# Optimization experiments

Hardware: AMD Instinct MI355X
Metric: run time of the kernel (lower is better)

The kernel has to match this reference:

```python
import jax, jax.numpy as jnp
import numpy as np
from jax import lax

N_NODES = 100000
D = 2048
E = 8192
H = 128
SIM_THRESHOLD = 0.7
EPS = 1e-8  # torch CosineSimilarity default eps


def setup_inputs() -> dict:
    key = jax.random.key(0)
    ks = jax.random.split(key, 8)
    x_idx = jax.random.randint(ks[0], (E,), 0, N_NODES, dtype=jnp.int32)
    y_idx = jax.random.randint(ks[1], (E,), 0, N_NODES, dtype=jnp.int32)
    x_feat = jax.random.normal(ks[2], (E, D), dtype=jnp.float32)
    y_feat = jax.random.normal(ks[3], (E, D), dtype=jnp.float32)
    # make ~half the pairs highly similar so the sim >= 0.7 branch is exercised
    coin = jax.random.uniform(ks[4], (E, 1)) < 0.5
    y_feat = jnp.where(coin, x_feat + 0.5 * y_feat, y_feat)
    W1 = 0.02 * jax.random.normal(ks[5], (H, 2 * D), dtype=jnp.float32)
    b1 = jnp.zeros((H,), jnp.float32)
    W2 = 0.02 * jax.random.normal(ks[6], (1, H), dtype=jnp.float32)
    b2 = jnp.zeros((1,), jnp.float32)
    parent = jnp.arange(N_NODES, dtype=jnp.int32)
    rank = jnp.ones((N_NODES,), jnp.float32)
    return {"x_idx": x_idx, "y_idx": y_idx, "x_feat": x_feat, "y_feat": y_feat,
            "W1": W1, "b1": b1, "W2": W2, "b2": b2,
            "parent": parent, "rank": rank}


def _gate(x_feat, y_feat, W1, b1, W2, b2):
    # cosine similarity with torch's eps clamp on each norm
    dot = jnp.sum(x_feat * y_feat, axis=-1)
    nx = jnp.maximum(jnp.sqrt(jnp.sum(x_feat * x_feat, axis=-1)), EPS)
    ny = jnp.maximum(jnp.sqrt(jnp.sum(y_feat * y_feat, axis=-1)), EPS)
    sim = dot / (nx * ny)
    h = jax.nn.relu(jnp.concatenate([x_feat, y_feat], axis=-1) @ W1.T + b1)  # [E, H]
    attn = jax.nn.sigmoid(h @ W2.T + b2)[:, 0]                               # [E]
    mask = sim >= SIM_THRESHOLD
    w = jnp.where(mask, attn, jnp.zeros_like(attn))
    return w, mask


def _find_root(parent, i):
    # iterative root find
    root = lax.while_loop(lambda r: parent[r] != r, lambda r: parent[r], i)
    # path compression: point every node on the path at root (matches recursive torch find)
    def comp_body(state):
        p, j = state
        nj = p[j]
        p = p.at[j].set(root)
        return p, nj
    parent, _ = lax.while_loop(lambda s: s[1] != root, comp_body, (parent, i))
    return parent, root


def reference(x_idx, y_idx, x_feat, y_feat, W1, b1, W2, b2, parent, rank):
    w, mask = _gate(x_feat, y_feat, W1, b1, W2, b2)

    def step(carry, inp):
        x, y, wi, m = inp
        def do(c):
            p, r = c
            p, rx = _find_root(p, x)
            p, ry = _find_root(p, y)
            bigger_x = r[rx] > r[ry]
            big = jnp.where(bigger_x, rx, ry)
            small = jnp.where(bigger_x, ry, rx)
            same = rx == ry
            # if roots are equal: no structural change, no rank update
            p = p.at[jnp.where(same, big, small)].set(big)
            r = r.at[big].add(jnp.where(same, 0.0, r[small] * wi))
            return p, r
        carry = lax.cond(m, do, lambda c: c, carry)
        return carry, None

    (parent, rank), _ = lax.scan(step, (parent, rank), (x_idx, y_idx, w, mask))
    return w, parent, rank
```

## Files before the change

kernel.cpp:

```cpp
#include <hip/hip_runtime.h>
#include <math.h>

#define E_EDGES 8192
#define D_FEAT 2048
#define K2 4096
#define H_DIM 128
#define N_NODES 100000
#define SIM_TH 0.7f
#define NSLOTS (2 * E_EDGES)
#define GBM 16

__global__ __launch_bounds__(256) void sim_kernel(const float* __restrict__ xf,
                                                  const float* __restrict__ yf,
                                                  float* __restrict__ sim) {
    int gid  = blockIdx.x * blockDim.x + threadIdx.x;
    int wave = gid >> 6;
    int lane = threadIdx.x & 63;
    if (wave >= E_EDGES) return;
    const float4* xp = (const float4*)(xf + (size_t)wave * D_FEAT);
    const float4* yp = (const float4*)(yf + (size_t)wave * D_FEAT);
    float dot = 0.f, xx = 0.f, yy = 0.f;
#pragma unroll
    for (int j = 0; j < 8; ++j) {
        float4 a = xp[lane + j * 64];
        float4 b = yp[lane + j * 64];
        dot += a.x * b.x + a.y * b.y + a.z * b.z + a.w * b.w;
        xx  += a.x * a.x + a.y * a.y + a.z * a.z + a.w * a.w;
        yy  += b.x * b.x + b.y * b.y + b.z * b.z + b.w * b.w;
    }
#pragma unroll
    for (int off = 32; off; off >>= 1) {
        dot += __shfl_xor(dot, off);
        xx  += __shfl_xor(xx, off);
        yy  += __shfl_xor(yy, off);
    }
    if (lane == 0) {
        float nx = fmaxf(sqrtf(xx), 1e-8f);
        float ny = fmaxf(sqrtf(yy), 1e-8f);
        sim[wave] = dot / (nx * ny);
    }
}

__global__ void initmap_kernel(int* __restrict__ fo, int* __restrict__ orig,
                               float* __restrict__ wout) {
    int i = blockIdx.x * blockDim.x + threadIdx.x;
    if (i < N_NODES) fo[i] = 0x7FFFFFFF;
    if (i < NSLOTS)  orig[i] = -1;
    if (i < E_EDGES) wout[i] = 0.f;
}

__global__ void claim_kernel(const int* __restrict__ x_idx, const int* __restrict__ y_idx,
                             int* __restrict__ fo) {
    int i = blockIdx.x * blockDim.x + threadIdx.x;
    if (i >= NSLOTS) return;
    int e = i >> 1;
    int v = (i & 1) ? y_idx[e] : x_idx[e];
    atomicMin(&fo[v], i);
}

__global__ void orig_kernel(const int* __restrict__ x_idx, const int* __restrict__ y_idx,
                            const int* __restrict__ fo, int* __restrict__ orig) {
    int i = blockIdx.x * blockDim.x + threadIdx.x;
    if (i >= NSLOTS) return;
    int e = i >> 1;
    int v = (i & 1) ? y_idx[e] : x_idx[e];
    if (fo[v] == i) orig[i] = v;
}

__global__ __launch_bounds__(256) void maskscan_kernel(
        const int* __restrict__ x_idx, const int* __restrict__ y_idx,
        const int* __restrict__ fo, const float* __restrict__ sim,
        int4* __restrict__ rec, int* __restrict__ nmask) {
    __shared__ int partial[256];
    int t = threadIdx.x;
    int cnt = 0;
    for (int j = 0; j < 32; ++j) {
        int e = t * 32 + j;
        cnt += (sim[e] >= SIM_TH) ? 1 : 0;
    }
    partial[t] = cnt;
    __syncthreads();
    for (int off = 1; off < 256; off <<= 1) {
        int mine  = partial[t];
        int other = (t >= off) ? partial[t - off] : 0;
        __syncthreads();
        partial[t] = mine + other;
        __syncthreads();
    }
    int pos = partial[t] - cnt;
    if (t == 255) {
        int nn = partial[255];
        *nmask = nn;
        for (int j = 0; j < 4; ++j) rec[nn + j] = make_int4(0, 0, 0, 0);
    }
    for (int j = 0; j < 32; ++j) {
        int e = t * 32 + j;
        if (sim[e] >= SIM_TH) {
            int4 r;
            r.x = fo[x_idx[e]];
            r.y = fo[y_idx[e]];
            r.z = e;
            r.w = 0;
            rec[pos++] = r;
        }
    }
}

__global__ __launch_bounds__(256) void gate_split_kernel(
        const float* __restrict__ xf, const float* __restrict__ yf,
        const float* __restrict__ W1,
        const int4* __restrict__ rec, const int* __restrict__ nmask,
        float* __restrict__ pbuf) {
    __shared__ float As[2][GBM][32];
    __shared__ float Bs[2][H_DIM][33];
    __shared__ int   elds[GBM];

    int n  = *nmask;
    int b0 = blockIdx.x * GBM;
    if (b0 >= n) return;
    const int h = blockIdx.y;

    int t = threadIdx.x;
    if (t < GBM) {
        int idx = b0 + t;
        elds[t] = (idx < n) ? rec[idx].z : rec[b0].z;
    }
    __syncthreads();

    const int  arow = t >> 3;
    const int  acol = (t & 7) * 4;
    const bool aact = (t < 128);
    const int  brow = t >> 3;
    const int  bcol = (t & 7) * 4;

    const float* feat = h ? yf : xf;
    const float* arp  = feat + (size_t)elds[aact ? arow : 0] * D_FEAT + acol;
    const size_t koff = (size_t)h * D_FEAT;
    const float* w1p0 = W1 + (size_t)(brow +  0) * K2 + koff + bcol;
    const float* w1p1 = W1 + (size_t)(brow + 32) * K2 + koff + bcol;
    const float* w1p2 = W1 + (size_t)(brow + 64) * K2 + koff + bcol;
    const float* w1p3 = W1 + (size_t)(brow + 96) * K2 + koff + bcol;

    float4 aR = make_float4(0.f, 0.f, 0.f, 0.f);
    float4 bR0, bR1, bR2, bR3;

    if (aact) aR = *(const float4*)(arp + 0);
    bR0 = *(const float4*)(w1p0 + 0);
    bR1 = *(const float4*)(w1p1 + 0);
    bR2 = *(const float4*)(w1p2 + 0);
    bR3 = *(const float4*)(w1p3 + 0);
    if (aact) *(float4*)(&As[0][arow][acol]) = aR;
    Bs[0][brow +  0][bcol + 0] = bR0.x; Bs[0][brow +  0][bcol + 1] = bR0.y;
    Bs[0][brow +  0][bcol + 2] = bR0.z; Bs[0][brow +  0][bcol + 3] = bR0.w;
    Bs[0][brow + 32][bcol + 0] = bR1.x; Bs[0][brow + 32][bcol + 1] = bR1.y;
    Bs[0][brow + 32][bcol + 2] = bR1.z; Bs[0][brow + 32][bcol + 3] = bR1.w;
    Bs[0][brow + 64][bcol + 0] = bR2.x; Bs[0][brow + 64][bcol + 1] = bR2.y;
    Bs[0][brow + 64][bcol + 2] = bR2.z; Bs[0][brow + 64][bcol + 3] = bR2.w;
    Bs[0][brow + 96][bcol + 0] = bR3.x; Bs[0][brow + 96][bcol + 1] = bR3.y;
    Bs[0][brow + 96][bcol + 2] = bR3.z; Bs[0][brow + 96][bcol + 3] = bR3.w;
    __syncthreads();

    const int eb = (t >> 6) * 4;
    const int ln = t & 63;
    float acc[4][2] = {{0.f,0.f},{0.f,0.f},{0.f,0.f},{0.f,0.f}};

    const int NT = D_FEAT / 32;
    for (int tile = 0; tile < NT; ++tile) {
        const int buf = tile & 1;
        if (tile + 1 < NT) {
            int k0 = (tile + 1) * 32;
            if (aact) aR = *(const float4*)(arp + k0);
            bR0 = *(const float4*)(w1p0 + k0);
            bR1 = *(const float4*)(w1p1 + k0);
            bR2 = *(const float4*)(w1p2 + k0);
            bR3 = *(const float4*)(w1p3 + k0);
        }
#pragma unroll
        for (int kk = 0; kk < 32; kk += 4) {
            float4 a0 = *(const float4*)(&As[buf][eb + 0][kk]);
            float4 a1 = *(const float4*)(&As[buf][eb + 1][kk]);
            float4 a2 = *(const float4*)(&As[buf][eb + 2][kk]);
            float4 a3 = *(const float4*)(&As[buf][eb + 3][kk]);
            float bl0 = Bs[buf][ln][kk + 0];
            float bl1 = Bs[buf][ln][kk + 1];
            float bl2 = Bs[buf][ln][kk + 2];
            float bl3 = Bs[buf][ln][kk + 3];
            float bh0 = Bs[buf][ln + 64][kk + 0];
            float bh1 = Bs[buf][ln + 64][kk + 1];
            float bh2 = Bs[buf][ln + 64][kk + 2];
            float bh3 = Bs[buf][ln + 64][kk + 3];
            acc[0][0] = fmaf(a0.x, bl0, acc[0][0]);
            acc[0][0] = fmaf(a0.y, bl1, acc[0][0]);
            acc[0][0] = fmaf(a0.z, bl2, acc[0][0]);
            acc[0][0] = fmaf(a0.w, bl3, acc[0][0]);
            acc[0][1] = fmaf(a0.x, bh0, acc[0][1]);
            acc[0][1] = fmaf(a0.y, bh1, acc[0][1]);
            acc[0][1] = fmaf(a0.z, bh2, acc[0][1]);
            acc[0][1] = fmaf(a0.w, bh3, acc[0][1]);
            acc[1][0] = fmaf(a1.x, bl0, acc[1][0]);
            acc[1][0] = fmaf(a1.y, bl1, acc[1][0]);
            acc[1][0] = fmaf(a1.z, bl2, acc[1][0]);
            acc[1][0] = fmaf(a1.w, bl3, acc[1][0]);
            acc[1][1] = fmaf(a1.x, bh0, acc[1][1]);
            acc[1][1] = fmaf(a1.y, bh1, acc[1][1]);
            acc[1][1] = fmaf(a1.z, bh2, acc[1][1]);
            acc[1][1] = fmaf(a1.w, bh3, acc[1][1]);
            acc[2][0] = fmaf(a2.x, bl0, acc[2][0]);
            acc[2][0] = fmaf(a2.y, bl1, acc[2][0]);
            acc[2][0] = fmaf(a2.z, bl2, acc[2][0]);
            acc[2][0] = fmaf(a2.w, bl3, acc[2][0]);
            acc[2][1] = fmaf(a2.x, bh0, acc[2][1]);
            acc[2][1] = fmaf(a2.y, bh1, acc[2][1]);
            acc[2][1] = fmaf(a2.z, bh2, acc[2][1]);
            acc[2][1] = fmaf(a2.w, bh3, acc[2][1]);
            acc[3][0] = fmaf(a3.x, bl0, acc[3][0]);
            acc[3][0] = fmaf(a3.y, bl1, acc[3][0]);
            acc[3][0] = fmaf(a3.z, bl2, acc[3][0]);
            acc[3][0] = fmaf(a3.w, bl3, acc[3][0]);
            acc[3][1] = fmaf(a3.x, bh0, acc[3][1]);
            acc[3][1] = fmaf(a3.y, bh1, acc[3][1]);
            acc[3][1] = fmaf(a3.z, bh2, acc[3][1]);
            acc[3][1] = fmaf(a3.w, bh3, acc[3][1]);
        }
        if (tile + 1 < NT) {
            const int nb = buf ^ 1;
            if (aact) *(float4*)(&As[nb][arow][acol]) = aR;
            Bs[nb][brow +  0][bcol + 0] = bR0.x; Bs[nb][brow +  0][bcol + 1] = bR0.y;
            Bs[nb][brow +  0][bcol + 2] = bR0.z; Bs[nb][brow +  0][bcol + 3] = bR0.w;
            Bs[nb][brow + 32][bcol + 0] = bR1.x; Bs[nb][brow + 32][bcol + 1] = bR1.y;
            Bs[nb][brow + 32][bcol + 2] = bR1.z; Bs[nb][brow + 32][bcol + 3] = bR1.w;
            Bs[nb][brow + 64][bcol + 0] = bR2.x; Bs[nb][brow + 64][bcol + 1] = bR2.y;
            Bs[nb][brow + 64][bcol + 2] = bR2.z; Bs[nb][brow + 64][bcol + 3] = bR2.w;
            Bs[nb][brow + 96][bcol + 0] = bR3.x; Bs[nb][brow + 96][bcol + 1] = bR3.y;
            Bs[nb][brow + 96][bcol + 2] = bR3.z; Bs[nb][brow + 96][bcol + 3] = bR3.w;
        }
        __syncthreads();
    }

#pragma unroll
    for (int j = 0; j < 4; ++j) {
        float* pb = pbuf + (((size_t)(b0 + eb + j) * 2 + h) << 7);
        pb[ln]      = acc[j][0];
        pb[ln + 64] = acc[j][1];
    }
}

__global__ __launch_bounds__(256) void gate_fin_kernel(
        const float* __restrict__ pbuf, const float* __restrict__ b1,
        const float* __restrict__ W2, const float* __restrict__ b2,
        int4* __restrict__ rec, const int* __restrict__ nmask,
        float* __restrict__ wout) {
    int e = blockIdx.x * blockDim.x + threadIdx.x;
    if (e >= *nmask) return;
    const float* p0 = pbuf + ((size_t)e << 8);
    const float* p1 = p0 + 128;
    float s = 0.f;
    for (int c = 0; c < 32; ++c) {
        float p = 0.f;
#pragma unroll
        for (int q = 0; q < 4; ++q) {
            int nn = 4 * c + q;
            float hh = fmaxf(p0[nn] + p1[nn] + b1[nn], 0.f);
            p = fmaf(hh, W2[nn], p);
        }
        s += p;
    }
    float logit = s + b2[0];
    float attn  = 1.f / (1.f + expf(-logit));
    wout[rec[e].z] = attn;
    ((int*)&rec[e])[3] = __float_as_int(attn);
}

__global__ __launch_bounds__(256) void gate_v3_kernel(
        const float* __restrict__ xf, const float* __restrict__ yf,
        const float* __restrict__ W1, const float* __restrict__ b1,
        const float* __restrict__ W2, const float* __restrict__ b2,
        int4* __restrict__ rec, const int* __restrict__ nmask,
        float* __restrict__ wout) {
    __shared__ float As[2][GBM][32];
    __shared__ float Bs[2][H_DIM][33];
    __shared__ float hbuf[GBM][132];
    __shared__ int   elds[GBM];

    int n  = *nmask;
    int b0 = blockIdx.x * GBM;
    if (b0 >= n) return;

    int t = threadIdx.x;
    if (t < GBM) {
        int idx = b0 + t;
        elds[t] = (idx < n) ? rec[idx].z : rec[b0].z;
    }
    __syncthreads();

    const int  arow = t >> 3;
    const int  acol = (t & 7) * 4;
    const bool aact = (t < 128);
    const int  brow = t >> 3;
    const int  bcol = (t & 7) * 4;

    const float* xrow = xf + (size_t)elds[aact ? arow : 0] * D_FEAT + acol;
    const float* yrow = yf + (size_t)elds[aact ? arow : 0] * D_FEAT + acol;
    const float* w1p0 = W1 + (size_t)(brow +  0) * K2 + bcol;
    const float* w1p1 = W1 + (size_t)(brow + 32) * K2 + bcol;
    const float* w1p2 = W1 + (size_t)(brow + 64) * K2 + bcol;
    const float* w1p3 = W1 + (size_t)(brow + 96) * K2 + bcol;

    float4 aR = make_float4(0.f, 0.f, 0.f, 0.f);
    float4 bR0, bR1, bR2, bR3;

    if (aact) aR = *(const float4*)(xrow + 0);
    bR0 = *(const float4*)(w1p0 + 0);
    bR1 = *(const float4*)(w1p1 + 0);
    bR2 = *(const float4*)(w1p2 + 0);
    bR3 = *(const float4*)(w1p3 + 0);
    if (aact) *(float4*)(&As[0][arow][acol]) = aR;
    Bs[0][brow +  0][bcol + 0] = bR0.x; Bs[0][brow +  0][bcol + 1] = bR0.y;
    Bs[0][brow +  0][bcol + 2] = bR0.z; Bs[0][brow +  0][bcol + 3] = bR0.w;
    Bs[0][brow + 32][bcol + 0] = bR1.x; Bs[0][brow + 32][bcol + 1] = bR1.y;
    Bs[0][brow + 32][bcol + 2] = bR1.z; Bs[0][brow + 32][bcol + 3] = bR1.w;
    Bs[0][brow + 64][bcol + 0] = bR2.x; Bs[0][brow + 64][bcol + 1] = bR2.y;
    Bs[0][brow + 64][bcol + 2] = bR2.z; Bs[0][brow + 64][bcol + 3] = bR2.w;
    Bs[0][brow + 96][bcol + 0] = bR3.x; Bs[0][brow + 96][bcol + 1] = bR3.y;
    Bs[0][brow + 96][bcol + 2] = bR3.z; Bs[0][brow + 96][bcol + 3] = bR3.w;
    __syncthreads();

    const int eb = (t >> 6) * 4;
    const int ln = t & 63;
    float acc[4][2] = {{0.f,0.f},{0.f,0.f},{0.f,0.f},{0.f,0.f}};

    const int NT = K2 / 32;
    for (int tile = 0; tile < NT; ++tile) {
        const int buf = tile & 1;
        if (tile + 1 < NT) {
            int k0 = (tile + 1) * 32;
            if (aact) {
                const float* ap = (k0 < D_FEAT) ? (xrow + k0) : (yrow + (k0 - D_FEAT));
                aR = *(const float4*)ap;
            }
            bR0 = *(const float4*)(w1p0 + k0);
            bR1 = *(const float4*)(w1p1 + k0);
            bR2 = *(const float4*)(w1p2 + k0);
            bR3 = *(const float4*)(w1p3 + k0);
        }
#pragma unroll
        for (int kk = 0; kk < 32; kk += 4) {
            float4 a0 = *(const float4*)(&As[buf][eb + 0][kk]);
            float4 a1 = *(const float4*)(&As[buf][eb + 1][kk]);
            float4 a2 = *(const float4*)(&As[buf][eb + 2][kk]);
            float4 a3 = *(const float4*)(&As[buf][eb + 3][kk]);
            float bl0 = Bs[buf][ln][kk + 0];
            float bl1 = Bs[buf][ln][kk + 1];
            float bl2 = Bs[buf][ln][kk + 2];
            float bl3 = Bs[buf][ln][kk + 3];
            float bh0 = Bs[buf][ln + 64][kk + 0];
            float bh1 = Bs[buf][ln + 64][kk + 1];
            float bh2 = Bs[buf][ln + 64][kk + 2];
            float bh3 = Bs[buf][ln + 64][kk + 3];
            acc[0][0] = fmaf(a0.x, bl0, acc[0][0]);
            acc[0][0] = fmaf(a0.y, bl1, acc[0][0]);
            acc[0][0] = fmaf(a0.z, bl2, acc[0][0]);
            acc[0][0] = fmaf(a0.w, bl3, acc[0][0]);
            acc[0][1] = fmaf(a0.x, bh0, acc[0][1]);
            acc[0][1] = fmaf(a0.y, bh1, acc[0][1]);
            acc[0][1] = fmaf(a0.z, bh2, acc[0][1]);
            acc[0][1] = fmaf(a0.w, bh3, acc[0][1]);
            acc[1][0] = fmaf(a1.x, bl0, acc[1][0]);
            acc[1][0] = fmaf(a1.y, bl1, acc[1][0]);
            acc[1][0] = fmaf(a1.z, bl2, acc[1][0]);
            acc[1][0] = fmaf(a1.w, bl3, acc[1][0]);
            acc[1][1] = fmaf(a1.x, bh0, acc[1][1]);
            acc[1][1] = fmaf(a1.y, bh1, acc[1][1]);
            acc[1][1] = fmaf(a1.z, bh2, acc[1][1]);
            acc[1][1] = fmaf(a1.w, bh3, acc[1][1]);
            acc[2][0] = fmaf(a2.x, bl0, acc[2][0]);
            acc[2][0] = fmaf(a2.y, bl1, acc[2][0]);
            acc[2][0] = fmaf(a2.z, bl2, acc[2][0]);
            acc[2][0] = fmaf(a2.w, bl3, acc[2][0]);
            acc[2][1] = fmaf(a2.x, bh0, acc[2][1]);
            acc[2][1] = fmaf(a2.y, bh1, acc[2][1]);
            acc[2][1] = fmaf(a2.z, bh2, acc[2][1]);
            acc[2][1] = fmaf(a2.w, bh3, acc[2][1]);
            acc[3][0] = fmaf(a3.x, bl0, acc[3][0]);
            acc[3][0] = fmaf(a3.y, bl1, acc[3][0]);
            acc[3][0] = fmaf(a3.z, bl2, acc[3][0]);
            acc[3][0] = fmaf(a3.w, bl3, acc[3][0]);
            acc[3][1] = fmaf(a3.x, bh0, acc[3][1]);
            acc[3][1] = fmaf(a3.y, bh1, acc[3][1]);
            acc[3][1] = fmaf(a3.z, bh2, acc[3][1]);
            acc[3][1] = fmaf(a3.w, bh3, acc[3][1]);
        }
        if (tile + 1 < NT) {
            const int nb = buf ^ 1;
            if (aact) *(float4*)(&As[nb][arow][acol]) = aR;
            Bs[nb][brow +  0][bcol + 0] = bR0.x; Bs[nb][brow +  0][bcol + 1] = bR0.y;
            Bs[nb][brow +  0][bcol + 2] = bR0.z; Bs[nb][brow +  0][bcol + 3] = bR0.w;
            Bs[nb][brow + 32][bcol + 0] = bR1.x; Bs[nb][brow + 32][bcol + 1] = bR1.y;
            Bs[nb][brow + 32][bcol + 2] = bR1.z; Bs[nb][brow + 32][bcol + 3] = bR1.w;
            Bs[nb][brow + 64][bcol + 0] = bR2.x; Bs[nb][brow + 64][bcol + 1] = bR2.y;
            Bs[nb][brow + 64][bcol + 2] = bR2.z; Bs[nb][brow + 64][bcol + 3] = bR2.w;
            Bs[nb][brow + 96][bcol + 0] = bR3.x; Bs[nb][brow + 96][bcol + 1] = bR3.y;
            Bs[nb][brow + 96][bcol + 2] = bR3.z; Bs[nb][brow + 96][bcol + 3] = bR3.w;
        }
        __syncthreads();
    }

#pragma unroll
    for (int j = 0; j < 4; ++j) {
        hbuf[eb + j][ln]      = fmaxf(acc[j][0] + b1[ln], 0.f);
        hbuf[eb + j][ln + 64] = fmaxf(acc[j][1] + b1[ln + 64], 0.f);
    }
    __syncthreads();
    if (t < GBM && b0 + t < n) {
        float s = 0.f;
        for (int c = 0; c < 32; ++c) {
            float p = 0.f;
#pragma unroll
            for (int q = 0; q < 4; ++q)
                p = fmaf(hbuf[t][4 * c + q], W2[4 * c + q], p);
            s += p;
        }
        float logit = s + b2[0];
        float attn  = 1.f / (1.f + expf(-logit));
        wout[elds[t]] = attn;
        ((int*)&rec[b0 + t])[3] = __float_as_int(attn);
    }
}

__global__ __launch_bounds__(1024) void label_kernel(
        const int4* __restrict__ rec, const int* __restrict__ nmask,
        int* __restrict__ elab) {
    extern __shared__ int L[];
    int t = threadIdx.x;
    int n = *nmask;
    for (int c = t; c < NSLOTS; c += 1024) L[c] = c;
    __syncthreads();
    for (;;) {
        if (t == 0) L[NSLOTS] = 0;
        __syncthreads();
        for (int e = t; e < n; e += 1024) {
            int4 r = rec[e];
            int a = L[r.x], b = L[r.y];
            if (a < b)      { atomicMin(&L[r.y], a); L[NSLOTS] = 1; }
            else if (b < a) { atomicMin(&L[r.x], b); L[NSLOTS] = 1; }
        }
        __syncthreads();
        if (!L[NSLOTS]) break;
        __syncthreads();
        for (int c = t; c < NSLOTS; c += 1024) {
            int q  = L[c];
            int qq = L[q];
            if (qq < q) L[c] = qq;
        }
        __syncthreads();
    }
    __syncthreads();
    for (int e = t; e < n; e += 1024) elab[e] = L[rec[e].x];
}

__global__ __launch_bounds__(1024) void radix_kernel(
        int4* __restrict__ bufA, int4* __restrict__ bufB,
        int* __restrict__ keyA, int* __restrict__ keyB,
        const int* __restrict__ nmask,
        int* __restrict__ compStart, int* __restrict__ ncompOut) {
    __shared__ int F[16384];
    __shared__ int P[1024];
    int t = threadIdx.x;
    int n = *nmask;
    int c = (n + 1023) >> 10;

    for (int pass = 0; pass < 4; ++pass) {
        int sh = pass * 4;
        const int4* in   = (pass & 1) ? bufB : bufA;
        int4*       out  = (pass & 1) ? bufA : bufB;
        const int*  kin  = (pass & 1) ? keyB : keyA;
        int*        kout = (pass & 1) ? keyA : keyB;
        for (int q = 0; q < 16; ++q) F[t * 16 + q] = 0;
        __syncthreads();
        for (int j = 0; j < c; ++j) {
            int i = t * c + j;
            if (i < n) {
                int d = (kin[i] >> sh) & 15;
                F[d * 1024 + t] += 1;
            }
        }
        __syncthreads();
        int base = t * 16;
        int loc[16]; int s = 0;
#pragma unroll
        for (int q = 0; q < 16; ++q) { loc[q] = s; s += F[base + q]; }
        P[t] = s;
        __syncthreads();
        for (int off = 1; off < 1024; off <<= 1) {
            int mine  = P[t];
            int other = (t >= off) ? P[t - off] : 0;
            __syncthreads();
            P[t] = mine + other;
            __syncthreads();
        }
        int pre = (t == 0) ? 0 : P[t - 1];
#pragma unroll
        for (int q = 0; q < 16; ++q) F[base + q] = pre + loc[q];
        __syncthreads();
        for (int j = 0; j < c; ++j) {
            int i = t * c + j;
            if (i < n) {
                int k = kin[i];
                int d = (k >> sh) & 15;
                int pos = F[d * 1024 + t]++;
                out[pos]  = in[i];
                kout[pos] = k;
            }
        }
        __syncthreads();
    }

    unsigned char* hd = (unsigned char*)F;
    for (int i = t; i < n; i += 1024) {
        int l  = keyA[i];
        int lp = (i == 0) ? -1 : keyA[i - 1];
        hd[i] = (l != lp) ? 1 : 0;
    }
    __syncthreads();
    int hsum = 0;
    for (int j = 0; j < c; ++j) {
        int i = t * c + j;
        if (i < n) hsum += hd[i];
    }
    P[t] = hsum;
    __syncthreads();
    for (int off = 1; off < 1024; off <<= 1) {
        int mine  = P[t];
        int other = (t >= off) ? P[t - off] : 0;
        __syncthreads();
        P[t] = mine + other;
        __syncthreads();
    }
    int run = P[t] - hsum;
    for (int j = 0; j < c; ++j) {
        int i = t * c + j;
        if (i < n && hd[i]) { compStart[run] = i; ++run; }
    }
    if (t == 1023) { int total = P[1023]; *ncompOut = total; compStart[total] = n; }
}

__global__ __launch_bounds__(1024) void uf_kernel(
        const int4* __restrict__ srec, const int* __restrict__ ncompPtr,
        const int* __restrict__ compStart,
        const int* __restrict__ orig, const float* __restrict__ rin,
        int* __restrict__ gpar, float* __restrict__ grank) {
    extern __shared__ char smem[];
    int2* nd = (int2*)smem;
    int* ndw = (int*)smem;
    int t = threadIdx.x;
    for (int c = t; c < NSLOTS; c += 1024) {
        int o = orig[c];
        float r = (o >= 0) ? rin[o] : 1.0f;
        nd[c] = make_int2(c, __float_as_int(r));
    }
    __syncthreads();

    int ncomp = *ncompPtr;
    for (int c = t; c < ncomp; c += 1024) {
        int s  = compStart[c];
        int en = compStart[c + 1];
        for (int j = s; j < en; ++j) {
            int4 r = srec[j];
            int x = r.x, y = r.y;
            float wi = __int_as_float(r.w);
            int p;
            int rx = x;
            while ((p = ndw[rx * 2]) != rx) rx = p;
            int j2 = x;
            while ((p = ndw[j2 * 2]) != rx) { ndw[j2 * 2] = rx; j2 = p; }
            int ry = y;
            while ((p = ndw[ry * 2]) != ry) ry = p;
            j2 = y;
            while ((p = ndw[j2 * 2]) != ry) { ndw[j2 * 2] = ry; j2 = p; }
            if (rx != ry) {
                float ka = __int_as_float(ndw[rx * 2 + 1]);
                float kb = __int_as_float(ndw[ry * 2 + 1]);
                bool bx = ka > kb;
                int big = bx ? rx : ry, small = bx ? ry : rx;
                float nr = bx ? (ka + kb * wi) : (kb + ka * wi);
                ndw[small * 2]   = big;
                ndw[big * 2 + 1] = __float_as_int(nr);
            }
        }
    }
    __syncthreads();
    for (int c = t; c < NSLOTS; c += 1024) {
        int2 v = nd[c];
        gpar[c] = v.x;
        grank[c] = __int_as_float(v.y);
    }
}

__global__ void finalize_kernel(const int* __restrict__ pin, const float* __restrict__ rin,
                                const int* __restrict__ fo, const int* __restrict__ orig,
                                const int* __restrict__ gpar, const float* __restrict__ grank,
                                float* __restrict__ pout, float* __restrict__ rout) {
    int i = blockIdx.x * blockDim.x + threadIdx.x;
    if (i >= N_NODES) return;
    int c = fo[i];
    float pv, rv;
    if (c != 0x7FFFFFFF) {
        pv = (float)orig[gpar[c]];
        rv = grank[c];
    } else {
        pv = (float)pin[i];
        rv = rin[i];
    }
    pout[i] = pv;
    rout[i] = rv;
}

extern "C" void kernel_launch(void* const* d_in, const int* in_sizes, int n_in,
                              void* d_out, int out_size, void* d_ws, size_t ws_size,
                              hipStream_t stream) {
    const int*   x_idx = (const int*)d_in[0];
    const int*   y_idx = (const int*)d_in[1];
    const float* xf    = (const float*)d_in[2];
    const float* yf    = (const float*)d_in[3];
    const float* W1    = (const float*)d_in[4];
    const float* b1    = (const float*)d_in[5];
    const float* W2    = (const float*)d_in[6];
    const float* b2    = (const float*)d_in[7];
    const int*   pin   = (const int*)d_in[8];
    const float* rin   = (const float*)d_in[9];

    float* out   = (float*)d_out;
    float* w_out = out;
    float* pout  = out + E_EDGES;
    float* rout  = out + E_EDGES + N_NODES;

    char* ws = (char*)d_ws;
    float* sim_ws  = (float*)(ws + 0);
    int*   fo      = (int*)  (ws + 32768);
    int*   orig    = (int*)  (ws + 432768);
    int4*  rec     = (int4*) (ws + 498304);
    int*   nmask   = (int*)  (ws + 629440);
    int*   gpar    = (int*)  (ws + 629504);
    float* grank   = (float*)(ws + 695040);
    int4*  srec    = (int4*) (ws + 760576);
    int*   keyB    = (int*)  (ws + 891648);
    int*   compSt  = (int*)  (ws + 924416);
    int*   ncomp   = (int*)  (ws + 957188);
    float* pbuf    = (float*)(ws + 957440);
    int*   keyA    = (int*)sim_ws;

    const size_t need_split = 957440 + (size_t)E_EDGES * 256 * sizeof(float);

    sim_kernel<<<(E_EDGES * 64) / 256, 256, 0, stream>>>(xf, yf, sim_ws);
    int g = (N_NODES + 255) / 256;
    initmap_kernel<<<g, 256, 0, stream>>>(fo, orig, w_out);
    claim_kernel<<<NSLOTS / 256, 256, 0, stream>>>(x_idx, y_idx, fo);
    orig_kernel<<<NSLOTS / 256, 256, 0, stream>>>(x_idx, y_idx, fo, orig);
    maskscan_kernel<<<1, 256, 0, stream>>>(x_idx, y_idx, fo, sim_ws, rec, nmask);
    if (ws_size >= need_split) {
        dim3 gg(E_EDGES / GBM, 2);
        gate_split_kernel<<<gg, 256, 0, stream>>>(xf, yf, W1, rec, nmask, pbuf);
        gate_fin_kernel<<<E_EDGES / 256, 256, 0, stream>>>(pbuf, b1, W2, b2,
                                                           rec, nmask, w_out);
    } else {
        gate_v3_kernel<<<E_EDGES / GBM, 256, 0, stream>>>(xf, yf, W1, b1, W2, b2,
                                                          rec, nmask, w_out);
    }
    label_kernel<<<1, 1024, (NSLOTS + 1) * sizeof(int), stream>>>(rec, nmask, keyA);
    radix_kernel<<<1, 1024, 0, stream>>>(rec, srec, keyA, keyB, nmask, compSt, ncomp);
    uf_kernel<<<1, 1024, 131072, stream>>>(rec, ncomp, compSt, orig, rin, gpar, grank);
    finalize_kernel<<<g, 256, 0, stream>>>(pin, rin, fo, orig, gpar, grank, pout, rout);
}
```

Baseline: 267.8 us.

## Fuse mask compaction, component labeling and radix sort into one kernel

Merges the mask-scan, label-propagation and radix-sort kernels into a single 1024-thread block. That block keeps the sort keys and label array in LDS instead of global memory, and it now runs before the gate GEMM. The aim is to cut two kernel launches and the global round-trips of the key and label arrays on this serial single-block path. It needs about 136 KB of dynamic LDS. The gate now works on records already sorted by component, and it still writes each attention value back into its record.

```diff
diff --git a/kernel.cpp b/kernel.cpp
--- a/kernel.cpp
+++ b/kernel.cpp
@@ -67,34 +67,44 @@
     if (fo[v] == i) orig[i] = v;
 }
 
-__global__ __launch_bounds__(256) void maskscan_kernel(
+__global__ __launch_bounds__(1024) void sortprep_kernel(
         const int* __restrict__ x_idx, const int* __restrict__ y_idx,
         const int* __restrict__ fo, const float* __restrict__ sim,
-        int4* __restrict__ rec, int* __restrict__ nmask) {
-    __shared__ int partial[256];
+        int4* __restrict__ rec, int4* __restrict__ srec,
+        int* __restrict__ nmask, int* __restrict__ compStart,
+        int* __restrict__ ncompOut) {
+    extern __shared__ char sm[];
+    int* keys0 = (int*)sm;
+    int* keys1 = (int*)(sm + 32768);
+    int* C     = (int*)(sm + 65536);
+    int* P     = (int*)(sm + 131072);
     int t = threadIdx.x;
+
     int cnt = 0;
-    for (int j = 0; j < 32; ++j) {
-        int e = t * 32 + j;
+#pragma unroll
+    for (int j = 0; j < 8; ++j) {
+        int e = t * 8 + j;
         cnt += (sim[e] >= SIM_TH) ? 1 : 0;
     }
-    partial[t] = cnt;
-    __syncthreads();
-    for (int off = 1; off < 256; off <<= 1) {
-        int mine  = partial[t];
-        int other = (t >= off) ? partial[t - off] : 0;
-        __syncthreads();
-        partial[t] = mine + other;
-        __syncthreads();
-    }
-    int pos = partial[t] - cnt;
-    if (t == 255) {
-        int nn = partial[255];
-        *nmask = nn;
+    P[t] = cnt;
+    __syncthreads();
+    for (int off = 1; off < 1024; off <<= 1) {
+        int mine  = P[t];
+        int other = (t >= off) ? P[t - off] : 0;
+        __syncthreads();
+        P[t] = mine + other;
+        __syncthreads();
+    }
+    int pos = P[t] - cnt;
+    if (t == 1023) {
+        int nn = P[1023];
+        *nmask  = nn;
+        P[1501] = nn;
         for (int j = 0; j < 4; ++j) rec[nn + j] = make_int4(0, 0, 0, 0);
     }
-    for (int j = 0; j < 32; ++j) {
-        int e = t * 32 + j;
+#pragma unroll
+    for (int j = 0; j < 8; ++j) {
+        int e = t * 8 + j;
         if (sim[e] >= SIM_TH) {
             int4 r;
             r.x = fo[x_idx[e]];
@@ -104,6 +114,111 @@
             rec[pos++] = r;
         }
     }
+    __syncthreads();
+    const int n = P[1501];
+
+    int* L = C;
+    for (int c = t; c < NSLOTS; c += 1024) L[c] = c;
+    __syncthreads();
+    for (;;) {
+        if (t == 0) P[1500] = 0;
+        __syncthreads();
+        for (int e = t; e < n; e += 1024) {
+            int4 r = rec[e];
+            int a = L[r.x], b = L[r.y];
+            if (a < b)      { atomicMin(&L[r.y], a); P[1500] = 1; }
+            else if (b < a) { atomicMin(&L[r.x], b); P[1500] = 1; }
+        }
+        __syncthreads();
+        if (!P[1500]) break;
+        __syncthreads();
+        for (int c = t; c < NSLOTS; c += 1024) {
+            int q  = L[c];
+            int qq = L[q];
+            if (qq < q) L[c] = qq;
+        }
+        __syncthreads();
+    }
+    __syncthreads();
+    for (int e = t; e < n; e += 1024) keys0[e] = L[rec[e].x];
+    __syncthreads();
+
+    int* F = C;
+    const int c8 = (n + 1023) >> 10;
+    for (int pass = 0; pass < 4; ++pass) {
+        int sh = pass * 4;
+        const int*  kin  = (pass & 1) ? keys1 : keys0;
+        int*        kout = (pass & 1) ? keys0 : keys1;
+        const int4* in   = (pass & 1) ? srec : rec;
+        int4*       out  = (pass & 1) ? rec : srec;
+#pragma unroll
+        for (int q = 0; q < 16; ++q) F[t * 16 + q] = 0;
+        __syncthreads();
+        for (int j = 0; j < c8; ++j) {
+            int i = t * c8 + j;
+            if (i < n) {
+                int d = (kin[i] >> sh) & 15;
+                F[d * 1024 + t] += 1;
+            }
+        }
+        __syncthreads();
+        int base = t * 16;
+        int loc[16]; int s = 0;
+#pragma unroll
+        for (int q = 0; q < 16; ++q) { loc[q] = s; s += F[base + q]; }
+        P[t] = s;
+        __syncthreads();
+        for (int off = 1; off < 1024; off <<= 1) {
+            int mine  = P[t];
+            int other = (t >= off) ? P[t - off] : 0;
+            __syncthreads();
+            P[t] = mine + other;
+            __syncthreads();
+        }
+        int pre = (t == 0) ? 0 : P[t - 1];
+#pragma unroll
+        for (int q = 0; q < 16; ++q) F[base + q] = pre + loc[q];
+        __syncthreads();
+        for (int j = 0; j < c8; ++j) {
+            int i = t * c8 + j;
+            if (i < n) {
+                int k = kin[i];
+                int d = (k >> sh) & 15;
+                int pp = F[d * 1024 + t]++;
+                out[pp]  = in[i];
+                kout[pp] = k;
+            }
+        }
+        __syncthreads();
+    }
+
+    unsigned char* hd = (unsigned char*)C;
+    for (int i = t; i < n; i += 1024) {
+        int l  = keys0[i];
+        int lp = (i == 0) ? -1 : keys0[i - 1];
+        hd[i] = (l != lp) ? 1 : 0;
+    }
+    __syncthreads();
+    int hsum = 0;
+    for (int j = 0; j < c8; ++j) {
+        int i = t * c8 + j;
+        if (i < n) hsum += hd[i];
+    }
+    P[t] = hsum;
+    __syncthreads();
+    for (int off = 1; off < 1024; off <<= 1) {
+        int mine  = P[t];
+        int other = (t >= off) ? P[t - off] : 0;
+        __syncthreads();
+        P[t] = mine + other;
+        __syncthreads();
+    }
+    int run = P[t] - hsum;
+    for (int j = 0; j < c8; ++j) {
+        int i = t * c8 + j;
+        if (i < n && hd[i]) { compStart[run] = i; ++run; }
+    }
+    if (t == 1023) { int total = P[1023]; *ncompOut = total; compStart[total] = n; }
 }
 
 __global__ __launch_bounds__(256) void gate_split_kernel(
@@ -427,123 +542,6 @@
     }
 }
 
-__global__ __launch_bounds__(1024) void label_kernel(
-        const int4* __restrict__ rec, const int* __restrict__ nmask,
-        int* __restrict__ elab) {
-    extern __shared__ int L[];
-    int t = threadIdx.x;
-    int n = *nmask;
-    for (int c = t; c < NSLOTS; c += 1024) L[c] = c;
-    __syncthreads();
-    for (;;) {
-        if (t == 0) L[NSLOTS] = 0;
-        __syncthreads();
-        for (int e = t; e < n; e += 1024) {
-            int4 r = rec[e];
-            int a = L[r.x], b = L[r.y];
-            if (a < b)      { atomicMin(&L[r.y], a); L[NSLOTS] = 1; }
-            else if (b < a) { atomicMin(&L[r.x], b); L[NSLOTS] = 1; }
-        }
-        __syncthreads();
-        if (!L[NSLOTS]) break;
-        __syncthreads();
-        for (int c = t; c < NSLOTS; c += 1024) {
-            int q  = L[c];
-            int qq = L[q];
-            if (qq < q) L[c] = qq;
-        }
-        __syncthreads();
-    }
-    __syncthreads();
-    for (int e = t; e < n; e += 1024) elab[e] = L[rec[e].x];
-}
-
-__global__ __launch_bounds__(1024) void radix_kernel(
-        int4* __restrict__ bufA, int4* __restrict__ bufB,
-        int* __restrict__ keyA, int* __restrict__ keyB,
-        const int* __restrict__ nmask,
-        int* __restrict__ compStart, int* __restrict__ ncompOut) {
-    __shared__ int F[16384];
-    __shared__ int P[1024];
-    int t = threadIdx.x;
-    int n = *nmask;
-    int c = (n + 1023) >> 10;
-
-    for (int pass = 0; pass < 4; ++pass) {
-        int sh = pass * 4;
-        const int4* in   = (pass & 1) ? bufB : bufA;
-        int4*       out  = (pass & 1) ? bufA : bufB;
-        const int*  kin  = (pass & 1) ? keyB : keyA;
-        int*        kout = (pass & 1) ? keyA : keyB;
-        for (int q = 0; q < 16; ++q) F[t * 16 + q] = 0;
-        __syncthreads();
-        for (int j = 0; j < c; ++j) {
-            int i = t * c + j;
-            if (i < n) {
-                int d = (kin[i] >> sh) & 15;
-                F[d * 1024 + t] += 1;
-            }
-        }
-        __syncthreads();
-        int base = t * 16;
-        int loc[16]; int s = 0;
-#pragma unroll
-        for (int q = 0; q < 16; ++q) { loc[q] = s; s += F[base + q]; }
-        P[t] = s;
-        __syncthreads();
-        for (int off = 1; off < 1024; off <<= 1) {
-            int mine  = P[t];
-            int other = (t >= off) ? P[t - off] : 0;
-            __syncthreads();
-            P[t] = mine + other;
-            __syncthreads();
-        }
-        int pre = (t == 0) ? 0 : P[t - 1];
-#pragma unroll
-        for (int q = 0; q < 16; ++q) F[base + q] = pre + loc[q];
-        __syncthreads();
-        for (int j = 0; j < c; ++j) {
-            int i = t * c + j;
-            if (i < n) {
-                int k = kin[i];
-                int d = (k >> sh) & 15;
-                int pos = F[d * 1024 + t]++;
-                out[pos]  = in[i];
-                kout[pos] = k;
-            }
-        }
-        __syncthreads();
-    }
-
-    unsigned char* hd = (unsigned char*)F;
-    for (int i = t; i < n; i += 1024) {
-        int l  = keyA[i];
-        int lp = (i == 0) ? -1 : keyA[i - 1];
-        hd[i] = (l != lp) ? 1 : 0;
-    }
-    __syncthreads();
-    int hsum = 0;
-    for (int j = 0; j < c; ++j) {
-        int i = t * c + j;
-        if (i < n) hsum += hd[i];
-    }
-    P[t] = hsum;
-    __syncthreads();
-    for (int off = 1; off < 1024; off <<= 1) {
-        int mine  = P[t];
-        int other = (t >= off) ? P[t - off] : 0;
-        __syncthreads();
-        P[t] = mine + other;
-        __syncthreads();
-    }
-    int run = P[t] - hsum;
-    for (int j = 0; j < c; ++j) {
-        int i = t * c + j;
-        if (i < n && hd[i]) { compStart[run] = i; ++run; }
-    }
-    if (t == 1023) { int total = P[1023]; *ncompOut = total; compStart[total] = n; }
-}
-
 __global__ __launch_bounds__(1024) void uf_kernel(
         const int4* __restrict__ srec, const int* __restrict__ ncompPtr,
         const int* __restrict__ compStart,
@@ -643,21 +641,20 @@
     int*   gpar    = (int*)  (ws + 629504);
     float* grank   = (float*)(ws + 695040);
     int4*  srec    = (int4*) (ws + 760576);
-    int*   keyB    = (int*)  (ws + 891648);
-    int*   compSt  = (int*)  (ws + 924416);
-    int*   ncomp   = (int*)  (ws + 957188);
-    float* pbuf    = (float*)(ws + 957440);
-    int*   keyA    = (int*)sim_ws;
-
-    const size_t need_split = 957440 + (size_t)E_EDGES * 256 * sizeof(float);
+    int*   compSt  = (int*)  (ws + 891648);
+    int*   ncomp   = (int*)  (ws + 924424);
+    float* pbuf    = (float*)(ws + 924480);
+
+    const size_t need2 = 924480 + (size_t)E_EDGES * 2 * 128 * sizeof(float);
 
     sim_kernel<<<(E_EDGES * 64) / 256, 256, 0, stream>>>(xf, yf, sim_ws);
     int g = (N_NODES + 255) / 256;
     initmap_kernel<<<g, 256, 0, stream>>>(fo, orig, w_out);
     claim_kernel<<<NSLOTS / 256, 256, 0, stream>>>(x_idx, y_idx, fo);
     orig_kernel<<<NSLOTS / 256, 256, 0, stream>>>(x_idx, y_idx, fo, orig);
-    maskscan_kernel<<<1, 256, 0, stream>>>(x_idx, y_idx, fo, sim_ws, rec, nmask);
-    if (ws_size >= need_split) {
+    sortprep_kernel<<<1, 1024, 139264, stream>>>(x_idx, y_idx, fo, sim_ws,
+                                                 rec, srec, nmask, compSt, ncomp);
+    if (ws_size >= need2) {
         dim3 gg(E_EDGES / GBM, 2);
         gate_split_kernel<<<gg, 256, 0, stream>>>(xf, yf, W1, rec, nmask, pbuf);
         gate_fin_kernel<<<E_EDGES / 256, 256, 0, stream>>>(pbuf, b1, W2, b2,
@@ -666,8 +663,6 @@
         gate_v3_kernel<<<E_EDGES / GBM, 256, 0, stream>>>(xf, yf, W1, b1, W2, b2,
                                                           rec, nmask, w_out);
     }
-    label_kernel<<<1, 1024, (NSLOTS + 1) * sizeof(int), stream>>>(rec, nmask, keyA);
-    radix_kernel<<<1, 1024, 0, stream>>>(rec, srec, keyA, keyB, nmask, compSt, ncomp);
     uf_kernel<<<1, 1024, 131072, stream>>>(rec, ncomp, compSt, orig, rin, gpar, grank);
     finalize_kernel<<<g, 256, 0, stream>>>(pin, rin, fo, orig, gpar, grank, pout, rout);
 }
```

Result: slower. 274.5 us (+2.5%).
